# Kernel optimization log

Hardware: AMD Instinct MI355X
Metric: run time of the kernel (lower is better)

## Reference

```python
import jax, jax.numpy as jnp
import numpy as np
from jax.scipy.special import logsumexp

V, E, H, T, L = 50000, 256, 128, 64, 4096
D = int(np.log2(L))          # leaves live at heap level D
N = 2 * L - 1                # total nodes in perfect binary tree (heap indexing)


def _postorder(n_total):
    order = []
    def rec(i):
        if 2 * i + 1 < n_total:
            rec(2 * i + 1)
            rec(2 * i + 2)
        order.append(i)
    rec(0)
    return np.array(order, dtype=np.int32)

POST = _postorder(N)


def setup_inputs() -> dict:
    key = jax.random.key(0)
    ks = jax.random.split(key, 8)
    s = lambda k, shape, fan: (jax.random.normal(k, shape, jnp.float32) / np.sqrt(fan).astype(np.float32))
    return {
        "tokens": jax.random.randint(ks[0], (L,), 0, V),
        "emb": s(ks[1], (V, E), E),
        "W_ih": s(ks[2], (4 * H, E), E),
        "W_hh": s(ks[3], (4 * H, H), H),
        "b_ih": jnp.zeros((4 * H,), jnp.float32),
        "b_hh": jnp.zeros((4 * H,), jnp.float32),
        "W_p2h": s(ks[4], (H, 2 * H), 2 * H),
        "b_p2h": jnp.zeros((H,), jnp.float32),
        "W_uni": s(ks[5], (T, H), H),
        "b_uni": jnp.zeros((T,), jnp.float32),
        "W_edge": s(ks[6], (T * T, 2 * H), 2 * H),
        "b_edge": jnp.zeros((T * T,), jnp.float32),
    }


def reference(tokens, emb, W_ih, W_hh, b_ih, b_hh, W_p2h, b_p2h,
              W_uni, b_uni, W_edge, b_edge):
    # ---- Encoder: embedding + single-layer LSTM over the leaf sequence ----
    x = emb[tokens]                                   # [L, E]
    def step(carry, xt):
        h, c = carry
        g = W_ih @ xt + b_ih + W_hh @ h + b_hh        # torch gate order i,f,g,o
        i, f, gg, o = jnp.split(g, 4)
        c = jax.nn.sigmoid(f) * c + jax.nn.sigmoid(i) * jnp.tanh(gg)
        h = jax.nn.sigmoid(o) * jnp.tanh(c)
        return (h, c), h
    z = jnp.zeros((H,), x.dtype)
    _, leaf_h = jax.lax.scan(step, (z, z), x)         # [L, H]

    # ---- build_node_to_hidden: bottom-up per-level pair fusion ----
    hidden = jnp.zeros((N, H), x.dtype).at[L - 1:].set(leaf_h)
    for d in range(D - 1, -1, -1):
        idx = jnp.arange(2 ** d - 1, 2 ** (d + 1) - 1)
        pair = jnp.concatenate([hidden[2 * idx + 1], hidden[2 * idx + 2]], axis=1)
        hidden = hidden.at[idx].set(pair @ W_p2h.T + b_p2h)

    # ---- build_factors (batched over all nodes / edges) ----
    unary = hidden @ W_uni.T + b_uni                  # [N, T]
    child = jnp.arange(1, N)
    parent = (child - 1) // 2
    pair = jnp.concatenate([hidden[parent], hidden[child]], axis=1)
    edge_fac = (pair @ W_edge.T + b_edge).reshape(N - 1, T, T)  # edge (parent,child), idx = child-1

    # ---- upward pass (level-synchronous, bottom-up) ----
    v2f = unary                                       # node -> top factor message
    f2p = jnp.zeros((N, T), x.dtype)                  # factor -> parent message, indexed by child
    for d in range(D, -1, -1):
        idx = jnp.arange(2 ** d - 1, 2 ** (d + 1) - 1)
        if d < D:  # internal nodes: add both children's factor->node messages
            v2f = v2f.at[idx].add(f2p[2 * idx + 1] + f2p[2 * idx + 2])
        if d > 0:  # message through top edge factor to the parent
            f2p = f2p.at[idx].set(
                logsumexp(edge_fac[idx - 1] + v2f[idx][:, None, :], axis=2))

    # ---- downward pass (level-synchronous, top-down) ----
    f2n = jnp.zeros((N, T), x.dtype)                  # top-factor -> node message; root gets none
    for d in range(1, D + 1):
        idx = jnp.arange(2 ** d - 1, 2 ** (d + 1) - 1)
        par = (idx - 1) // 2
        sib = jnp.where(idx % 2 == 1, idx + 1, idx - 1)
        p2f = unary[par] + f2n[par] + f2p[sib]        # parent's messages, excluding this child's
        f2n = f2n.at[idx].set(
            logsumexp(edge_fac[idx - 1] + p2f[:, :, None], axis=1))

    beliefs = v2f + f2n                               # sum of all incoming messages, [N, T]
    return beliefs[POST]                              # stacked in postorder, like the original
```

## Files before the change

### kernel.cpp

```cpp
#include <hip/hip_runtime.h>
#include <hip/hip_bf16.h>

typedef __hip_bfloat16 bf16;
typedef float fx2 __attribute__((ext_vector_type(2)));

#define NL 4096
#define NH 128
#define NE 256
#define NT 64
#define NNODE 8191
#define NDEPTH 12

#define OF_WIH   0
#define OF_WHH   131072
#define OF_BIH   196608
#define OF_BHH   197120
#define OF_WP2H  197632
#define OF_BP2H  230400
#define OF_WUNI  230528
#define OF_BUNI  238720
#define OF_WEDGE 238784
#define OF_BEDGE 1287360
#define WF_TOTAL 1291456

__device__ __forceinline__ float b2f(bf16 x) { return __bfloat162float(x); }
__device__ __forceinline__ float blo(unsigned u) { return __uint_as_float(u << 16); }
__device__ __forceinline__ float bhi(unsigned u) { return __uint_as_float(u & 0xffff0000u); }

__global__ void detect_kernel(const void* __restrict__ wedge_raw, int* __restrict__ flag) {
  __shared__ int cnt_sh[256];
  const unsigned short* p = (const unsigned short*)wedge_raw;
  int c = 0;
  for (int i = threadIdx.x; i < 32768; i += 256) {
    float v = __uint_as_float(((unsigned)p[2 * i]) << 16);
    if (fabsf(v) > 4.f) c++;
  }
  cnt_sh[threadIdx.x] = c;
  __syncthreads();
  for (int s = 128; s > 0; s >>= 1) {
    if (threadIdx.x < s) cnt_sh[threadIdx.x] += cnt_sh[threadIdx.x + s];
    __syncthreads();
  }
  if (threadIdx.x == 0) *flag = cnt_sh[0];
}

__global__ void convert_kernel(const void* s0, const void* s1, const void* s2, const void* s3,
                               const void* s4, const void* s5, const void* s6, const void* s7,
                               const void* s8, const void* s9,
                               const int* __restrict__ flag, float* __restrict__ wf) {
  int i = blockIdx.x * 256 + threadIdx.x;
  if (i >= WF_TOTAL) return;
  const void* src; int local;
  if      (i < OF_WHH)   { src = s0; local = i; }
  else if (i < OF_BIH)   { src = s1; local = i - OF_WHH; }
  else if (i < OF_BHH)   { src = s2; local = i - OF_BIH; }
  else if (i < OF_WP2H)  { src = s3; local = i - OF_BHH; }
  else if (i < OF_BP2H)  { src = s4; local = i - OF_WP2H; }
  else if (i < OF_WUNI)  { src = s5; local = i - OF_BP2H; }
  else if (i < OF_BUNI)  { src = s6; local = i - OF_WUNI; }
  else if (i < OF_WEDGE) { src = s7; local = i - OF_BUNI; }
  else if (i < OF_BEDGE) { src = s8; local = i - OF_WEDGE; }
  else                   { src = s9; local = i - OF_BEDGE; }
  bool isf32 = (*flag) > 100;
  wf[i] = isf32 ? ((const float*)src)[local] : b2f(((const bf16*)src)[local]);
}

__global__ __launch_bounds__(512) void g1_kernel(const int* __restrict__ tokens,
                                                 const void* __restrict__ emb_raw,
                                                 const int* __restrict__ flag,
                                                 const float* __restrict__ wf,
                                                 float* __restrict__ G1) {
  __shared__ __attribute__((aligned(16))) float xs[8 * NE];
  const bool isf32 = (*flag) > 100;
  const int t0 = blockIdx.x * 8;
  for (int q = threadIdx.x; q < 8 * NE; q += 512) {
    int tok = q >> 8, e = q & 255;
    size_t off = (size_t)tokens[t0 + tok] * NE + e;
    xs[q] = isf32 ? ((const float*)emb_raw)[off] : b2f(((const bf16*)emb_raw)[off]);
  }
  __syncthreads();
  const int r = threadIdx.x;
  const float bias = wf[OF_BIH + r] + wf[OF_BHH + r];
  float acc[8];
#pragma unroll
  for (int k = 0; k < 8; ++k) acc[k] = bias;
  const float4* W4 = (const float4*)(wf + OF_WIH + (size_t)r * NE);
#pragma unroll 8
  for (int j = 0; j < 64; ++j) {
    float4 wv = W4[j];
#pragma unroll
    for (int tok = 0; tok < 8; ++tok) {
      float4 xv = ((const float4*)(xs + tok * NE))[j];
      acc[tok] += wv.x * xv.x + wv.y * xv.y + wv.z * xv.z + wv.w * xv.w;
    }
  }
#pragma unroll
  for (int tok = 0; tok < 8; ++tok) G1[(size_t)(t0 + tok) * 512 + r] = acc[tok];
}

__global__ __launch_bounds__(512) void lstm_kernel(const float* __restrict__ wf,
                                                   const void* __restrict__ whh_raw,
                                                   const int* __restrict__ flag,
                                                   const float* __restrict__ G1,
                                                   float* __restrict__ hidden) {
  const int r = threadIdx.x;
  __shared__ __attribute__((aligned(16))) float h_sh[NH];
  __shared__ float g_sh[512];
  const bool isf32 = (*flag) > 100;

  float c = 0.f;
  if (r < NH) h_sh[r] = 0.f;
  __syncthreads();
  float gnext = G1[r];

  if (!isf32) {
    const uint4* Wh = (const uint4*)((const unsigned short*)whh_raw + (size_t)r * NH);
    for (int t = 0; t < NL; ++t) {
      float gcur = gnext;
      if (t + 1 < NL) gnext = G1[(size_t)(t + 1) * 512 + r];
      const float4* h4 = (const float4*)h_sh;
      fx2 a0 = {0.f, 0.f}, a1 = {0.f, 0.f}, a2 = {0.f, 0.f}, a3 = {0.f, 0.f};
#pragma unroll
      for (int i = 0; i < 16; ++i) {
        uint4 wq = Wh[i];
        float4 hA = h4[2 * i], hB = h4[2 * i + 1];
        fx2 w01, w23, w45, w67, e01, e23, e45, e67;
        w01.x = blo(wq.x); w01.y = bhi(wq.x);
        w23.x = blo(wq.y); w23.y = bhi(wq.y);
        w45.x = blo(wq.z); w45.y = bhi(wq.z);
        w67.x = blo(wq.w); w67.y = bhi(wq.w);
        e01.x = hA.x; e01.y = hA.y; e23.x = hA.z; e23.y = hA.w;
        e45.x = hB.x; e45.y = hB.y; e67.x = hB.z; e67.y = hB.w;
        a0 += w01 * e01;
        a1 += w23 * e23;
        a2 += w45 * e45;
        a3 += w67 * e67;
      }
      g_sh[r] = gcur + (a0.x + a0.y) + (a1.x + a1.y) + (a2.x + a2.y) + (a3.x + a3.y);
      __syncthreads();
      if (r < NH) {
        float iv = g_sh[r], fv = g_sh[r + 128], gv = g_sh[r + 256], ov = g_sh[r + 384];
        float si = 1.f / (1.f + __expf(-iv));
        float sf = 1.f / (1.f + __expf(-fv));
        float tg = 1.f - 2.f / (__expf(2.f * gv) + 1.f);
        float so = 1.f / (1.f + __expf(-ov));
        c = sf * c + si * tg;
        float hh = so * (1.f - 2.f / (__expf(2.f * c) + 1.f));
        h_sh[r] = hh;
        hidden[(size_t)(NL - 1 + t) * NH + r] = hh;
      }
      __syncthreads();
    }
  } else {
    const float4* Wrow = (const float4*)(wf + OF_WHH + (size_t)r * NH);
    for (int t = 0; t < NL; ++t) {
      float gcur = gnext;
      if (t + 1 < NL) gnext = G1[(size_t)(t + 1) * 512 + r];
      const float4* h4 = (const float4*)h_sh;
      fx2 a0 = {0.f, 0.f}, a1 = {0.f, 0.f}, a2 = {0.f, 0.f}, a3 = {0.f, 0.f};
#pragma unroll
      for (int i = 0; i < 16; ++i) {
        float4 w0 = Wrow[2 * i], w1 = Wrow[2 * i + 1];
        float4 hA = h4[2 * i], hB = h4[2 * i + 1];
        fx2 u0, u1, u2, u3, e0, e1, e2, e3;
        u0.x = w0.x; u0.y = w0.y; u1.x = w0.z; u1.y = w0.w;
        u2.x = w1.x; u2.y = w1.y; u3.x = w1.z; u3.y = w1.w;
        e0.x = hA.x; e0.y = hA.y; e1.x = hA.z; e1.y = hA.w;
        e2.x = hB.x; e2.y = hB.y; e3.x = hB.z; e3.y = hB.w;
        a0 += u0 * e0;
        a1 += u1 * e1;
        a2 += u2 * e2;
        a3 += u3 * e3;
      }
      g_sh[r] = gcur + (a0.x + a0.y) + (a1.x + a1.y) + (a2.x + a2.y) + (a3.x + a3.y);
      __syncthreads();
      if (r < NH) {
        float iv = g_sh[r], fv = g_sh[r + 128], gv = g_sh[r + 256], ov = g_sh[r + 384];
        float si = 1.f / (1.f + __expf(-iv));
        float sf = 1.f / (1.f + __expf(-fv));
        float tg = 1.f - 2.f / (__expf(2.f * gv) + 1.f);
        float so = 1.f / (1.f + __expf(-ov));
        c = sf * c + si * tg;
        float hh = so * (1.f - 2.f / (__expf(2.f * c) + 1.f));
        h_sh[r] = hh;
        hidden[(size_t)(NL - 1 + t) * NH + r] = hh;
      }
      __syncthreads();
    }
  }
}

__global__ void p2h_kernel(const float* __restrict__ wf, float* __restrict__ hidden, int base) {
  int node = base + blockIdx.x;
  int j = threadIdx.x;
  __shared__ __attribute__((aligned(16))) float pr[2 * NH];
  const float* hl = hidden + (size_t)(2 * node + 1) * NH;
  pr[j] = hl[j];
  pr[j + NH] = hl[j + NH];
  __syncthreads();
  float acc = wf[OF_BP2H + j];
  const float4* W4 = (const float4*)(wf + OF_WP2H + (size_t)j * 2 * NH);
  const float4* p4 = (const float4*)pr;
#pragma unroll 16
  for (int q = 0; q < 64; ++q) {
    float4 u = W4[q], x = p4[q];
    acc += u.x * x.x + u.y * x.y + u.z * x.z + u.w * x.w;
  }
  hidden[(size_t)node * NH + j] = acc;
}

__global__ void unary_kernel(const float* __restrict__ wf, const float* __restrict__ hidden,
                             float* __restrict__ unary, float* __restrict__ f2n) {
  int node = blockIdx.x;
  int ct = threadIdx.x;
  __shared__ __attribute__((aligned(16))) float hs[NH];
  hs[ct] = hidden[(size_t)node * NH + ct];
  hs[ct + 64] = hidden[(size_t)node * NH + 64 + ct];
  __syncthreads();
  float acc = wf[OF_BUNI + ct];
  const float4* W4 = (const float4*)(wf + OF_WUNI + (size_t)ct * NH);
  const float4* h4 = (const float4*)hs;
#pragma unroll
  for (int q = 0; q < 32; ++q) {
    float4 u = W4[q], x = h4[q];
    acc += u.x * x.x + u.y * x.y + u.z * x.z + u.w * x.w;
  }
  unary[(size_t)node * NT + ct] = acc;
  if (node == 0) f2n[ct] = 0.f;
}

__global__ __launch_bounds__(256) void edge_kernel(const float* __restrict__ hidden,
                                                   const float* __restrict__ wf,
                                                   float* __restrict__ edge) {
  __shared__ __attribute__((aligned(16))) float As[32][132];
  __shared__ __attribute__((aligned(16))) float Bs[32][132];
  const int tid = threadIdx.x;
  const int nb = blockIdx.x;
  const int mb = blockIdx.y;
  const int tm = tid >> 4, tn = tid & 15;
  float acc[8][8];
#pragma unroll
  for (int i = 0; i < 8; ++i)
#pragma unroll
    for (int j = 0; j < 8; ++j) acc[i][j] = 0.f;
  const int sr = tid >> 1;
  const int sq = tid & 1;
  for (int ch = 0; ch < 8; ++ch) {
    {
      int gm = mb * 128 + sr;
      const float* srcA = (ch < 4) ? hidden + (size_t)(gm >> 1) * NH + ch * 32
                                   : hidden + (size_t)(gm + 1) * NH + (ch - 4) * 32;
      bool ok = (gm < NNODE - 1);
#pragma unroll
      for (int i = 0; i < 4; ++i) {
        int kk = sq * 16 + i * 4;
        float4 v = ok ? *(const float4*)(srcA + kk) : make_float4(0.f, 0.f, 0.f, 0.f);
        As[kk + 0][sr] = v.x; As[kk + 1][sr] = v.y; As[kk + 2][sr] = v.z; As[kk + 3][sr] = v.w;
      }
    }
    {
      int gn = nb * 128 + sr;
      const float* srcB = wf + OF_WEDGE + (size_t)gn * NE + ch * 32;
#pragma unroll
      for (int i = 0; i < 4; ++i) {
        int kk = sq * 16 + i * 4;
        float4 v = *(const float4*)(srcB + kk);
        Bs[kk + 0][sr] = v.x; Bs[kk + 1][sr] = v.y; Bs[kk + 2][sr] = v.z; Bs[kk + 3][sr] = v.w;
      }
    }
    __syncthreads();
#pragma unroll 8
    for (int kk = 0; kk < 32; ++kk) {
      float a[8], b[8];
      *(float4*)(a)     = *(const float4*)&As[kk][tm * 4];
      *(float4*)(a + 4) = *(const float4*)&As[kk][64 + tm * 4];
      *(float4*)(b)     = *(const float4*)&Bs[kk][tn * 4];
      *(float4*)(b + 4) = *(const float4*)&Bs[kk][64 + tn * 4];
#pragma unroll
      for (int i = 0; i < 8; ++i)
#pragma unroll
        for (int j = 0; j < 8; ++j) acc[i][j] += a[i] * b[j];
    }
    __syncthreads();
  }
  float bias[8];
#pragma unroll
  for (int j = 0; j < 8; ++j)
    bias[j] = wf[OF_BEDGE + nb * 128 + (j >> 2) * 64 + tn * 4 + (j & 3)];
#pragma unroll
  for (int i = 0; i < 8; ++i) {
    int gm = mb * 128 + (i >> 2) * 64 + tm * 4 + (i & 3);
    if (gm < NNODE - 1) {
      float* row = edge + (size_t)gm * 4096 + nb * 128;
      float4 o0, o1;
      o0.x = acc[i][0] + bias[0]; o0.y = acc[i][1] + bias[1];
      o0.z = acc[i][2] + bias[2]; o0.w = acc[i][3] + bias[3];
      o1.x = acc[i][4] + bias[4]; o1.y = acc[i][5] + bias[5];
      o1.z = acc[i][6] + bias[6]; o1.w = acc[i][7] + bias[7];
      *(float4*)(row + tn * 4) = o0;
      *(float4*)(row + 64 + tn * 4) = o1;
    }
  }
}

__global__ void up_kernel(const float* __restrict__ unary, const float* __restrict__ edge,
                          float* __restrict__ v2f, float* __restrict__ f2p,
                          int base, int depth) {
  int node = base + blockIdx.x;
  int tid = threadIdx.x;
  __shared__ __attribute__((aligned(16))) float vs[NT];
  float vv = unary[(size_t)node * NT + tid];
  if (depth < NDEPTH)
    vv += f2p[(size_t)(2 * node + 1) * NT + tid] + f2p[(size_t)(2 * node + 2) * NT + tid];
  v2f[(size_t)node * NT + tid] = vv;
  vs[tid] = vv;
  __syncthreads();
  if (depth == 0) return;
  const float4* E4 = (const float4*)(edge + (size_t)(node - 1) * 4096 + tid * 64);
  const float4* v4 = (const float4*)vs;
  float x[NT];
#pragma unroll
  for (int q = 0; q < 16; ++q) {
    float4 e = E4[q], vq = v4[q];
    x[4 * q + 0] = e.x + vq.x; x[4 * q + 1] = e.y + vq.y;
    x[4 * q + 2] = e.z + vq.z; x[4 * q + 3] = e.w + vq.w;
  }
  float m = x[0];
#pragma unroll
  for (int i = 1; i < NT; ++i) m = fmaxf(m, x[i]);
  float s = 0.f;
#pragma unroll
  for (int i = 0; i < NT; ++i) s += __expf(x[i] - m);
  f2p[(size_t)node * NT + tid] = m + __logf(s);
}

__global__ void down_kernel(const float* __restrict__ unary, const float* __restrict__ edge,
                            const float* __restrict__ f2p, float* __restrict__ f2n,
                            int base) {
  int node = base + blockIdx.x;
  int tid = threadIdx.x;
  int par = (node - 1) >> 1;
  int sib = (node & 1) ? node + 1 : node - 1;
  __shared__ __attribute__((aligned(16))) float us[NT];
  us[tid] = unary[(size_t)par * NT + tid] + f2n[(size_t)par * NT + tid] +
            f2p[(size_t)sib * NT + tid];
  __syncthreads();
  float uu[NT];
  const float4* u4 = (const float4*)us;
#pragma unroll
  for (int q = 0; q < 16; ++q) {
    float4 t4 = u4[q];
    uu[4 * q] = t4.x; uu[4 * q + 1] = t4.y; uu[4 * q + 2] = t4.z; uu[4 * q + 3] = t4.w;
  }
  const float* E = edge + (size_t)(node - 1) * 4096 + tid;
  float x[NT];
#pragma unroll
  for (int p = 0; p < NT; ++p) x[p] = E[(size_t)p * 64] + uu[p];
  float m = x[0];
#pragma unroll
  for (int i = 1; i < NT; ++i) m = fmaxf(m, x[i]);
  float s = 0.f;
#pragma unroll
  for (int i = 0; i < NT; ++i) s += __expf(x[i] - m);
  f2n[(size_t)node * NT + tid] = m + __logf(s);
}

__global__ void final_kernel(const float* __restrict__ v2f, const float* __restrict__ f2n,
                             const int* __restrict__ flag, void* __restrict__ out) {
  int node = blockIdx.x;
  int tid = threadIdx.x;
  unsigned v = (unsigned)node + 1u;
  int d = 31 - __clz((int)v);
  int b0 = 0, S = NNODE;
  for (int b = d - 1; b >= 0; --b) {
    int sz = (S - 1) >> 1;
    if ((v >> b) & 1) b0 += sz;
    S = sz;
  }
  int pos = b0 + S - 1;
  float val = v2f[(size_t)node * NT + tid] + f2n[(size_t)node * NT + tid];
  if ((*flag) > 100) ((float*)out)[(size_t)pos * NT + tid] = val;
  else               ((bf16*)out)[(size_t)pos * NT + tid] = __float2bfloat16(val);
}

extern "C" void kernel_launch(void* const* d_in, const int* in_sizes, int n_in,
                              void* d_out, int out_size, void* d_ws, size_t ws_size,
                              hipStream_t stream) {
  (void)in_sizes; (void)n_in; (void)out_size; (void)ws_size;
  const int* tokens = (const int*)d_in[0];

  float* ws     = (float*)d_ws;
  int*   flag   = (int*)ws;
  float* wf     = ws + 16;
  float* hidden = wf + WF_TOTAL;
  float* G1     = hidden + (size_t)NNODE * NH;
  float* unary  = G1 + (size_t)NL * 512;
  float* v2f    = unary + (size_t)NNODE * NT;
  float* f2p    = v2f + (size_t)NNODE * NT;
  float* f2n    = f2p + (size_t)NNODE * NT;
  float* edge   = f2n + (size_t)NNODE * NT;

  detect_kernel<<<1, 256, 0, stream>>>(d_in[10], flag);
  convert_kernel<<<(WF_TOTAL + 255) / 256, 256, 0, stream>>>(
      d_in[2], d_in[3], d_in[4], d_in[5], d_in[6], d_in[7],
      d_in[8], d_in[9], d_in[10], d_in[11], flag, wf);
  g1_kernel<<<NL / 8, 512, 0, stream>>>(tokens, d_in[1], flag, wf, G1);
  lstm_kernel<<<1, 512, 0, stream>>>(wf, d_in[3], flag, G1, hidden);
  for (int d = NDEPTH - 1; d >= 0; --d)
    p2h_kernel<<<1 << d, 128, 0, stream>>>(wf, hidden, (1 << d) - 1);
  unary_kernel<<<NNODE, 64, 0, stream>>>(wf, hidden, unary, f2n);
  edge_kernel<<<dim3(32, 64), 256, 0, stream>>>(hidden, wf, edge);
  for (int d = NDEPTH; d >= 0; --d)
    up_kernel<<<1 << d, 64, 0, stream>>>(unary, edge, v2f, f2p, (1 << d) - 1, d);
  for (int d = 1; d <= NDEPTH; ++d)
    down_kernel<<<1 << d, 64, 0, stream>>>(unary, edge, f2p, f2n, (1 << d) - 1);
  final_kernel<<<NNODE, 64, 0, stream>>>(v2f, f2n, flag, d_out);
}
```

Measured before the change: 4.035 ms.

## Remap LSTM gate rows to lanes and gather gates via shuffles

```diff
diff --git a/kernel.cpp b/kernel.cpp
--- a/kernel.cpp
+++ b/kernel.cpp
@@ -104,21 +104,24 @@
                                                    const float* __restrict__ G1,
                                                    float* __restrict__ hidden) {
   const int r = threadIdx.x;
-  __shared__ __attribute__((aligned(16))) float h_sh[NH];
-  __shared__ float g_sh[512];
+  const int q = r & 3;
+  const int j = r >> 2;
+  const int orow = q * 128 + j;
+  __shared__ __attribute__((aligned(16))) float h_sh[2][NH];
   const bool isf32 = (*flag) > 100;
 
   float c = 0.f;
-  if (r < NH) h_sh[r] = 0.f;
-  __syncthreads();
-  float gnext = G1[r];
+  if (r < NH) h_sh[0][r] = 0.f;
+  __syncthreads();
+  float gnext = G1[orow];
 
   if (!isf32) {
-    const uint4* Wh = (const uint4*)((const unsigned short*)whh_raw + (size_t)r * NH);
+    const uint4* Wh = (const uint4*)((const unsigned short*)whh_raw + (size_t)orow * NH);
     for (int t = 0; t < NL; ++t) {
       float gcur = gnext;
-      if (t + 1 < NL) gnext = G1[(size_t)(t + 1) * 512 + r];
-      const float4* h4 = (const float4*)h_sh;
+      if (t + 1 < NL) gnext = G1[(size_t)(t + 1) * 512 + orow];
+      const float4* h4 = (const float4*)h_sh[t & 1];
+      float* hn = h_sh[(t & 1) ^ 1];
       fx2 a0 = {0.f, 0.f}, a1 = {0.f, 0.f}, a2 = {0.f, 0.f}, a3 = {0.f, 0.f};
 #pragma unroll
       for (int i = 0; i < 16; ++i) {
@@ -136,27 +139,38 @@
         a2 += w45 * e45;
         a3 += w67 * e67;
       }
-      g_sh[r] = gcur + (a0.x + a0.y) + (a1.x + a1.y) + (a2.x + a2.y) + (a3.x + a3.y);
+      float gown = gcur + (a0.x + a0.y) + (a1.x + a1.y) + (a2.x + a2.y) + (a3.x + a3.y);
+      float x1 = __shfl_xor(gown, 1);
+      float x2 = __shfl_xor(gown, 2);
+      float x3 = __shfl_xor(x1, 2);
+      bool b0 = (q & 1) != 0, b1 = (q & 2) != 0;
+      float t01 = b0 ? x1 : gown;
+      float t23 = b0 ? x3 : x2;
+      float f01 = b0 ? gown : x1;
+      float f23 = b0 ? x2 : x3;
+      float iv = b1 ? t23 : t01;
+      float fv = b1 ? f23 : f01;
+      float gv = b1 ? t01 : t23;
+      float ov = b1 ? f01 : f23;
+      float si = 1.f / (1.f + __expf(-iv));
+      float sf = 1.f / (1.f + __expf(-fv));
+      float tg = 1.f - 2.f / (__expf(2.f * gv) + 1.f);
+      float so = 1.f / (1.f + __expf(-ov));
+      c = sf * c + si * tg;
+      float hh = so * (1.f - 2.f / (__expf(2.f * c) + 1.f));
+      if (q == 0) {
+        hn[j] = hh;
+        hidden[(size_t)(NL - 1 + t) * NH + j] = hh;
+      }
       __syncthreads();
-      if (r < NH) {
-        float iv = g_sh[r], fv = g_sh[r + 128], gv = g_sh[r + 256], ov = g_sh[r + 384];
-        float si = 1.f / (1.f + __expf(-iv));
-        float sf = 1.f / (1.f + __expf(-fv));
-        float tg = 1.f - 2.f / (__expf(2.f * gv) + 1.f);
-        float so = 1.f / (1.f + __expf(-ov));
-        c = sf * c + si * tg;
-        float hh = so * (1.f - 2.f / (__expf(2.f * c) + 1.f));
-        h_sh[r] = hh;
-        hidden[(size_t)(NL - 1 + t) * NH + r] = hh;
-      }
-      __syncthreads();
     }
   } else {
-    const float4* Wrow = (const float4*)(wf + OF_WHH + (size_t)r * NH);
+    const float4* Wrow = (const float4*)(wf + OF_WHH + (size_t)orow * NH);
     for (int t = 0; t < NL; ++t) {
       float gcur = gnext;
-      if (t + 1 < NL) gnext = G1[(size_t)(t + 1) * 512 + r];
-      const float4* h4 = (const float4*)h_sh;
+      if (t + 1 < NL) gnext = G1[(size_t)(t + 1) * 512 + orow];
+      const float4* h4 = (const float4*)h_sh[t & 1];
+      float* hn = h_sh[(t & 1) ^ 1];
       fx2 a0 = {0.f, 0.f}, a1 = {0.f, 0.f}, a2 = {0.f, 0.f}, a3 = {0.f, 0.f};
 #pragma unroll
       for (int i = 0; i < 16; ++i) {
@@ -172,18 +186,28 @@
         a2 += u2 * e2;
         a3 += u3 * e3;
       }
-      g_sh[r] = gcur + (a0.x + a0.y) + (a1.x + a1.y) + (a2.x + a2.y) + (a3.x + a3.y);
-      __syncthreads();
-      if (r < NH) {
-        float iv = g_sh[r], fv = g_sh[r + 128], gv = g_sh[r + 256], ov = g_sh[r + 384];
-        float si = 1.f / (1.f + __expf(-iv));
-        float sf = 1.f / (1.f + __expf(-fv));
-        float tg = 1.f - 2.f / (__expf(2.f * gv) + 1.f);
-        float so = 1.f / (1.f + __expf(-ov));
-        c = sf * c + si * tg;
-        float hh = so * (1.f - 2.f / (__expf(2.f * c) + 1.f));
-        h_sh[r] = hh;
-        hidden[(size_t)(NL - 1 + t) * NH + r] = hh;
+      float gown = gcur + (a0.x + a0.y) + (a1.x + a1.y) + (a2.x + a2.y) + (a3.x + a3.y);
+      float x1 = __shfl_xor(gown, 1);
+      float x2 = __shfl_xor(gown, 2);
+      float x3 = __shfl_xor(x1, 2);
+      bool b0 = (q & 1) != 0, b1 = (q & 2) != 0;
+      float t01 = b0 ? x1 : gown;
+      float t23 = b0 ? x3 : x2;
+      float f01 = b0 ? gown : x1;
+      float f23 = b0 ? x2 : x3;
+      float iv = b1 ? t23 : t01;
+      float fv = b1 ? f23 : f01;
+      float gv = b1 ? t01 : t23;
+      float ov = b1 ? f01 : f23;
+      float si = 1.f / (1.f + __expf(-iv));
+      float sf = 1.f / (1.f + __expf(-fv));
+      float tg = 1.f - 2.f / (__expf(2.f * gv) + 1.f);
+      float so = 1.f / (1.f + __expf(-ov));
+      c = sf * c + si * tg;
+      float hh = so * (1.f - 2.f / (__expf(2.f * c) + 1.f));
+      if (q == 0) {
+        hn[j] = hh;
+        hidden[(size_t)(NL - 1 + t) * NH + j] = hh;
       }
       __syncthreads();
     }
```

Result: slower. 4.428 ms (+9.7%).
